# Kernel optimization log

Hardware: AMD Instinct MI355X
Metric: run time of the kernel (lower is better)

Reference implementation:

```python
import jax, jax.numpy as jnp
import numpy as np

N = 100000      # nodes
E = 3200000     # edges
F_IN = 128      # dataset.num_features
H = 64          # hidden_channels
H2 = 32         # hidden_channels_2 (H//2); hidden_channels_3 unused by the module
C5 = 256        # 2 * num_features
NC = 6          # num_classes


def setup_inputs() -> dict:
    key = jax.random.key(0)
    ks = jax.random.split(key, 24)

    def w(k, fi, fo):
        return jax.random.normal(k, (fi, fo), jnp.float32) / np.float32(np.sqrt(fi))

    inp = {
        "x": jax.random.normal(ks[0], (N, F_IN), jnp.float32),
        "edge_index": jax.random.randint(ks[1], (2, E), 0, N, dtype=jnp.int32),
        "batch": jnp.zeros((N,), jnp.int32),
        # GCNConv weights/biases (conv_i: x @ W then normalized aggregation + b)
        "W1": w(ks[2], F_IN, H),  "b1": jnp.zeros((H,), jnp.float32),
        "W2": w(ks[3], H, H),     "b2": jnp.zeros((H,), jnp.float32),
        "W3": w(ks[4], H, H2),    "b3": jnp.zeros((H2,), jnp.float32),
        "W4": w(ks[5], H2, H2),   "b4": jnp.zeros((H2,), jnp.float32),
        "W5": w(ks[6], H2, C5),   "b5": jnp.zeros((C5,), jnp.float32),
        # Linear layers
        "Wl1": w(ks[7], C5, 24),  "bl1": jnp.zeros((24,), jnp.float32),
        "Wl2": w(ks[8], 24, 18),  "bl2": jnp.zeros((18,), jnp.float32),
        "Wl3": w(ks[9], 18, 12),  "bl3": jnp.zeros((12,), jnp.float32),
        "Wc":  w(ks[10], 24, NC), "bc": jnp.zeros((NC,), jnp.float32),
    }
    return inp


def reference(x, edge_index, batch,
              W1, b1, W2, b2, W3, b3, W4, b4, W5, b5,
              Wl1, bl1, Wl2, bl2, Wl3, bl3, Wc, bc):
    # --- GCN normalization (PyG GCNConv: add self loops, sym norm) ---
    loops = jnp.arange(N, dtype=edge_index.dtype)
    src = jnp.concatenate([edge_index[0], loops])   # message sources (x_j)
    dst = jnp.concatenate([edge_index[1], loops])   # aggregation targets
    deg = jax.ops.segment_sum(jnp.ones_like(dst, jnp.float32), dst, num_segments=N)
    dinv = jnp.where(deg > 0, jax.lax.rsqrt(jnp.maximum(deg, 1.0)), 0.0)
    norm = (dinv[src] * dinv[dst])[:, None]         # [E+N, 1]

    def gcn(h, W, b):
        m = (h @ W)[src] * norm
        return jax.ops.segment_sum(m, dst, num_segments=N) + b

    h = jnp.tanh(gcn(x, W1, b1))
    h = jnp.tanh(gcn(h, W2, b2))
    h = jnp.tanh(gcn(h, W3, b3))
    h = jnp.tanh(gcn(h, W4, b4))
    h = jnp.tanh(gcn(h, W5, b5))
    h = jnp.tanh(h @ Wl1 + bl1)
    h = jnp.tanh(h @ Wl2 + bl2)
    h = jnp.tanh(h @ Wl3 + bl3)                      # [N, 12]
    e = jnp.concatenate([h[edge_index[0]], h[edge_index[1]]], axis=1)  # [E, 24]
    out = e @ Wc + bc                                # [E, NC]
    return (out, e)
```

## Files before the change

### kernel.cpp

```cpp
#include <hip/hip_runtime.h>

typedef float f32x4 __attribute__((ext_vector_type(4)));
typedef float f32x2 __attribute__((ext_vector_type(2)));

constexpr int BKT_SHIFT = 7;
constexpr int NBKT_PAD  = 1024;
constexpr int CHUNK     = 8192;
constexpr int MAXSEG    = 6144;

__global__ __launch_bounds__(256) void k1_hist(const int* __restrict__ dst,
                                               int* __restrict__ Hist, int ne) {
    __shared__ int lh[NBKT_PAD];
    for (int i = threadIdx.x; i < NBKT_PAD; i += 256) lh[i] = 0;
    __syncthreads();
    int base = blockIdx.x * CHUNK;
    int lim = min(CHUNK, ne - base);
    for (int i = threadIdx.x; i < lim; i += 256)
        atomicAdd(&lh[dst[base + i] >> BKT_SHIFT], 1);
    __syncthreads();
    for (int i = threadIdx.x; i < NBKT_PAD; i += 256)
        Hist[(size_t)blockIdx.x * NBKT_PAD + i] = lh[i];
}

__global__ __launch_bounds__(128) void k2a_sum(const int* __restrict__ Hist,
                                               int* __restrict__ bucketTot, int nblk) {
    int b = blockIdx.x * 128 + threadIdx.x;
    int tot = 0;
    int blk = 0;
    for (; blk + 4 <= nblk; blk += 4)
        tot += Hist[(size_t)blk * NBKT_PAD + b] +
               Hist[(size_t)(blk + 1) * NBKT_PAD + b] +
               Hist[(size_t)(blk + 2) * NBKT_PAD + b] +
               Hist[(size_t)(blk + 3) * NBKT_PAD + b];
    for (; blk < nblk; ++blk) tot += Hist[(size_t)blk * NBKT_PAD + b];
    bucketTot[b] = tot;
}

__global__ __launch_bounds__(1024) void k2b_scan(const int* __restrict__ bucketTot,
                                                 int* __restrict__ bktBase,
                                                 int* __restrict__ row_ptrN) {
    __shared__ int wsums[16];
    int t = threadIdx.x, wave = t >> 6, lane = t & 63;
    int tot = bucketTot[t];
    int x = tot;
    #pragma unroll
    for (int off = 1; off < 64; off <<= 1) {
        int y = __shfl_up(x, off, 64);
        if (lane >= off) x += y;
    }
    if (lane == 63) wsums[wave] = x;
    __syncthreads();
    if (t < 16) {
        int w = wsums[t];
        #pragma unroll
        for (int off = 1; off < 16; off <<= 1) {
            int y = __shfl_up(w, off, 64);
            if (t >= off) w += y;
        }
        wsums[t] = w;
    }
    __syncthreads();
    int excl = (wave ? wsums[wave - 1] : 0) + (x - tot);
    bktBase[t] = excl;
    if (t == 1023) { bktBase[1024] = excl + tot; *row_ptrN = excl + tot; }
}

__global__ __launch_bounds__(128) void k2c_rewrite(int* __restrict__ Hist,
                                                   const int* __restrict__ bktBase, int nblk) {
    int b = blockIdx.x * 128 + threadIdx.x;
    int run = bktBase[b];
    for (int blk = 0; blk < nblk; ++blk) {
        size_t idx = (size_t)blk * NBKT_PAD + b;
        int v = Hist[idx];
        Hist[idx] = run;
        run += v;
    }
}

__global__ __launch_bounds__(256) void k3_partition(const int* __restrict__ src,
                                                    const int* __restrict__ dst,
                                                    const int* __restrict__ Hist,
                                                    int2* __restrict__ es, int ne) {
    __shared__ int cur[NBKT_PAD];
    for (int i = threadIdx.x; i < NBKT_PAD; i += 256)
        cur[i] = Hist[(size_t)blockIdx.x * NBKT_PAD + i];
    __syncthreads();
    int base = blockIdx.x * CHUNK;
    int lim = min(CHUNK, ne - base);
    for (int i = threadIdx.x; i < lim; i += 256) {
        int d = dst[base + i];
        int s = src[base + i];
        int pos = atomicAdd(&cur[d >> BKT_SHIFT], 1);
        es[pos] = make_int2(s, d);
    }
}

__global__ __launch_bounds__(256) void k4_csr(const int2* __restrict__ es,
                                              const int* __restrict__ bktBase,
                                              int* __restrict__ col_idx,
                                              int* __restrict__ row_ptr,
                                              float* __restrict__ dinv, int n) {
    __shared__ int hist[128];
    __shared__ int rbase[128];
    __shared__ int cur[128];
    __shared__ int stage[MAXSEG];
    int b = blockIdx.x;
    int segs = bktBase[b], sege = bktBase[b + 1];
    int seglen = sege - segs;
    int node0 = b << BKT_SHIFT;
    int nloc = min(128, n - node0);
    int t = threadIdx.x;
    if (t < 128) hist[t] = 0;
    __syncthreads();
    for (int i = t; i < seglen; i += 256)
        atomicAdd(&hist[es[segs + i].y - node0], 1);
    __syncthreads();
    if (t < 64) {
        int a0 = hist[2 * t], a1 = hist[2 * t + 1];
        int pair = a0 + a1;
        int x = pair;
        #pragma unroll
        for (int off = 1; off < 64; off <<= 1) {
            int y = __shfl_up(x, off, 64);
            if (t >= off) x += y;
        }
        int excl = x - pair;
        rbase[2 * t] = excl;       rbase[2 * t + 1] = excl + a0;
        cur[2 * t]   = excl;       cur[2 * t + 1]   = excl + a0;
    }
    __syncthreads();
    if (seglen <= MAXSEG) {
        for (int i = t; i < seglen; i += 256) {
            int2 e = es[segs + i];
            int pos = atomicAdd(&cur[e.y - node0], 1);
            stage[pos] = e.x;
        }
        __syncthreads();
        for (int i = t; i < seglen; i += 256)
            col_idx[segs + i] = stage[i];
    } else {
        for (int i = t; i < seglen; i += 256) {
            int2 e = es[segs + i];
            int pos = atomicAdd(&cur[e.y - node0], 1);
            col_idx[segs + pos] = e.x;
        }
    }
    if (t < nloc) {
        row_ptr[node0 + t] = segs + rbase[t];
        dinv[node0 + t] = 1.0f / sqrtf((float)(hist[t] + 1));
    }
}

template<int K, int FOUT, int EPI, int RT>
__global__ __launch_bounds__(256) void gemm_tiled(const float* __restrict__ X,
        const float* __restrict__ W, const float* __restrict__ bias,
        const float* __restrict__ dinv, float* __restrict__ Y, int nrows) {
    __shared__ float Wl[K * FOUT];
    __shared__ float Xs[RT * K];
    int tid = threadIdx.x;
    const float4* Wg4 = (const float4*)W;
    float4* Wl4 = (float4*)Wl;
    for (int i = tid; i < K * FOUT / 4; i += 256) Wl4[i] = Wg4[i];
    int row0 = blockIdx.x * RT;
    int nr = min(RT, nrows - row0);
    {
        const float4* Xg4 = (const float4*)(X + (size_t)row0 * K);
        float4* Xs4 = (float4*)Xs;
        int lim = nr * (K / 4);
        for (int i = tid; i < lim; i += 256) Xs4[i] = Xg4[i];
    }
    __syncthreads();

    constexpr int NG  = 256 / FOUT;
    constexpr int RPT = RT / NG;
    int c = tid & (FOUT - 1);
    int g = tid / FOUT;
    int rbase = g * RPT;
    float acc[RPT];
    #pragma unroll
    for (int i = 0; i < RPT; ++i) acc[i] = 0.f;
    #pragma unroll 4
    for (int k = 0; k < K; ++k) {
        float wv = Wl[k * FOUT + c];
        #pragma unroll
        for (int i = 0; i < RPT; ++i)
            acc[i] = fmaf(Xs[(rbase + i) * K + k], wv, acc[i]);
    }
    float bv = (EPI == 1) ? bias[c] : 0.f;
    #pragma unroll
    for (int i = 0; i < RPT; ++i) {
        int r = row0 + rbase + i;
        if (r < nrows) {
            float v = acc[i];
            if (EPI == 0) v *= dinv[r];
            else          v = tanhf(v + bv);
            Y[(size_t)r * FOUT + c] = v;
        }
    }
}

__global__ __launch_bounds__(256) void head_kernel(const float* __restrict__ X,
        const float* __restrict__ W5, const float* __restrict__ b5,
        const float* __restrict__ Wl1, const float* __restrict__ bl1,
        const float* __restrict__ Wl2, const float* __restrict__ bl2,
        const float* __restrict__ Wl3, const float* __restrict__ bl3,
        float* __restrict__ Y, int nrows) {
    constexpr int RT = 16;
    __shared__ float W5s[32 * 256];
    __shared__ float W1s[256 * 24];
    __shared__ float W2s[24 * 18];
    __shared__ float W3s[18 * 12];
    __shared__ float b1s[24], b2s[18], b3s[12];
    __shared__ float Xs[RT * 32];
    __shared__ float H5[RT * 257];
    __shared__ float H24[RT * 25];
    __shared__ float H18[RT * 19];
    int tid = threadIdx.x;
    for (int i = tid; i < 32 * 256 / 4; i += 256) ((float4*)W5s)[i] = ((const float4*)W5)[i];
    for (int i = tid; i < 256 * 24 / 4; i += 256) ((float4*)W1s)[i] = ((const float4*)Wl1)[i];
    for (int i = tid; i < 432; i += 256) W2s[i] = Wl2[i];
    for (int i = tid; i < 216; i += 256) W3s[i] = Wl3[i];
    if (tid < 24) b1s[tid] = bl1[tid];
    if (tid < 18) b2s[tid] = bl2[tid];
    if (tid < 12) b3s[tid] = bl3[tid];
    float b5r = b5[tid];
    int row0 = blockIdx.x * RT;
    int nr = min(RT, nrows - row0);
    {
        const float4* Xg4 = (const float4*)(X + (size_t)row0 * 32);
        for (int i = tid; i < nr * 8; i += 256) ((float4*)Xs)[i] = Xg4[i];
    }
    __syncthreads();
    {
        float acc[RT];
        #pragma unroll
        for (int r = 0; r < RT; ++r) acc[r] = 0.f;
        #pragma unroll 4
        for (int k = 0; k < 32; ++k) {
            float wv = W5s[k * 256 + tid];
            #pragma unroll
            for (int r = 0; r < RT; ++r)
                acc[r] = fmaf(Xs[r * 32 + k], wv, acc[r]);
        }
        #pragma unroll
        for (int r = 0; r < RT; ++r) H5[r * 257 + tid] = tanhf(acc[r] + b5r);
    }
    __syncthreads();
    for (int o = tid; o < RT * 24; o += 256) {
        int r = o / 24, c = o - r * 24;
        float acc = 0.f;
        #pragma unroll 4
        for (int k = 0; k < 256; ++k) acc = fmaf(H5[r * 257 + k], W1s[k * 24 + c], acc);
        H24[r * 25 + c] = tanhf(acc + b1s[c]);
    }
    __syncthreads();
    for (int o = tid; o < RT * 18; o += 256) {
        int r = o / 18, c = o - r * 18;
        float acc = 0.f;
        #pragma unroll
        for (int k = 0; k < 24; ++k) acc = fmaf(H24[r * 25 + k], W2s[k * 18 + c], acc);
        H18[r * 19 + c] = tanhf(acc + b2s[c]);
    }
    __syncthreads();
    for (int o = tid; o < RT * 12; o += 256) {
        int r = o / 12, c = o - r * 12;
        float acc = 0.f;
        #pragma unroll
        for (int k = 0; k < 18; ++k) acc = fmaf(H18[r * 19 + k], W3s[k * 12 + c], acc);
        if (r < nr) Y[(size_t)(row0 + r) * 12 + c] = tanhf(acc + b3s[c]);
    }
}

template<int F, bool FINAL, bool POSTSCALE>
__global__ __launch_bounds__(256) void aggregate_kernel(const float* __restrict__ Z,
        const int* __restrict__ row_ptr, const int* __restrict__ col_idx,
        const float* __restrict__ dinv, const float* __restrict__ bias,
        float* __restrict__ out, int n) {
    constexpr int LPR = F / 4;
    constexpr int G   = 64 / LPR;
    int tid = threadIdx.x;
    int wave = tid >> 6, lane = tid & 63;
    int g = lane / LPR;
    int c = lane - g * LPR;
    int node = blockIdx.x * 4 + wave;
    if (node >= n) return;
    int start = row_ptr[node];
    int end   = row_ptr[node + 1];
    float4 acc = make_float4(0.f, 0.f, 0.f, 0.f);
    int wbase = start;
    int iv = (wbase + lane < end) ? col_idx[wbase + lane] : 0;
    #pragma unroll 2
    for (int base = start; base < end; base += G) {
        if (base - wbase == 64) {
            wbase += 64;
            iv = (wbase + lane < end) ? col_idx[wbase + lane] : 0;
        }
        int s = __shfl(iv, (base - wbase) + g, 64);
        if (base + g < end) {
            const float4 v = *(const float4*)(Z + (size_t)s * F + c * 4);
            acc.x += v.x; acc.y += v.y; acc.z += v.z; acc.w += v.w;
        }
    }
    #pragma unroll
    for (int off = LPR; off < 64; off <<= 1) {
        acc.x += __shfl_xor(acc.x, off, 64);
        acc.y += __shfl_xor(acc.y, off, 64);
        acc.z += __shfl_xor(acc.z, off, 64);
        acc.w += __shfl_xor(acc.w, off, 64);
    }
    if (g == 0) {
        const float4 sv = *(const float4*)(Z + (size_t)node * F + c * 4);
        float di = dinv[node];
        float4 r;
        r.x = di * (acc.x + sv.x);
        r.y = di * (acc.y + sv.y);
        r.z = di * (acc.z + sv.z);
        r.w = di * (acc.w + sv.w);
        if (FINAL) {
            const float4 bv = *(const float4*)(bias + c * 4);
            r.x = tanhf(r.x + bv.x);
            r.y = tanhf(r.y + bv.y);
            r.z = tanhf(r.z + bv.z);
            r.w = tanhf(r.w + bv.w);
        }
        if (POSTSCALE) { r.x *= di; r.y *= di; r.z *= di; r.w *= di; }
        *(float4*)(out + (size_t)node * F + c * 4) = r;
    }
}

__global__ __launch_bounds__(256) void edge_kernel(const int* __restrict__ src,
        const int* __restrict__ dst, const float* __restrict__ h,
        const float* __restrict__ Wc, const float* __restrict__ bc,
        float* __restrict__ out, float* __restrict__ efeat, int ne) {
    __shared__ float Wl[144];
    __shared__ float bl[6];
    if (threadIdx.x < 144) Wl[threadIdx.x] = Wc[threadIdx.x];
    if (threadIdx.x < 6) bl[threadIdx.x] = bc[threadIdx.x];
    __syncthreads();
    int e = blockIdx.x * 256 + threadIdx.x;
    if (e >= ne) return;
    int s = src[e], d = dst[e];
    const float* hs = h + (size_t)s * 12;
    const float* hd = h + (size_t)d * 12;
    f32x4 v0 = *(const f32x4*)(hs + 0);
    f32x4 v1 = *(const f32x4*)(hs + 4);
    f32x4 v2 = *(const f32x4*)(hs + 8);
    f32x4 v3 = *(const f32x4*)(hd + 0);
    f32x4 v4 = *(const f32x4*)(hd + 4);
    f32x4 v5 = *(const f32x4*)(hd + 8);
    float v[24];
    *(f32x4*)(v + 0)  = v0; *(f32x4*)(v + 4)  = v1; *(f32x4*)(v + 8)  = v2;
    *(f32x4*)(v + 12) = v3; *(f32x4*)(v + 16) = v4; *(f32x4*)(v + 20) = v5;
    f32x4* ef4 = (f32x4*)(efeat + (size_t)e * 24);
    ef4[0] = v0; ef4[1] = v1; ef4[2] = v2; ef4[3] = v3; ef4[4] = v4; ef4[5] = v5;
    float o[6];
    #pragma unroll
    for (int c = 0; c < 6; ++c) {
        float acc = bl[c];
        #pragma unroll
        for (int k = 0; k < 24; ++k) acc = fmaf(v[k], Wl[k * 6 + c], acc);
        o[c] = acc;
    }
    f32x2* o2 = (f32x2*)(out + (size_t)e * 6);
    f32x2 p0; p0.x = o[0]; p0.y = o[1];
    f32x2 p1; p1.x = o[2]; p1.y = o[3];
    f32x2 p2; p2.x = o[4]; p2.y = o[5];
    o2[0] = p0; o2[1] = p1; o2[2] = p2;
}

extern "C" void kernel_launch(void* const* d_in, const int* in_sizes, int n_in,
                              void* d_out, int out_size, void* d_ws, size_t ws_size,
                              hipStream_t stream) {
    const int N = in_sizes[0] / 128;
    const int E = in_sizes[1] / 2;

    const float* x   = (const float*)d_in[0];
    const int*   ei  = (const int*)d_in[1];
    const int*   srcE = ei;
    const int*   dstE = ei + E;
    const float* W1 = (const float*)d_in[3];  const float* b1 = (const float*)d_in[4];
    const float* W2 = (const float*)d_in[5];  const float* b2 = (const float*)d_in[6];
    const float* W3 = (const float*)d_in[7];  const float* b3 = (const float*)d_in[8];
    const float* W4 = (const float*)d_in[9];  const float* b4 = (const float*)d_in[10];
    const float* W5 = (const float*)d_in[11]; const float* b5 = (const float*)d_in[12];
    const float* Wl1 = (const float*)d_in[13]; const float* bl1 = (const float*)d_in[14];
    const float* Wl2 = (const float*)d_in[15]; const float* bl2 = (const float*)d_in[16];
    const float* Wl3 = (const float*)d_in[17]; const float* bl3 = (const float*)d_in[18];
    const float* Wc  = (const float*)d_in[19]; const float* bc  = (const float*)d_in[20];

    char* ws = (char*)d_ws;
    size_t off = 0;
    auto take = [&](size_t bytes) -> char* {
        char* p = ws + off;
        off += (bytes + 255) & ~(size_t)255;
        return p;
    };
    int*   row_ptr   = (int*)take((size_t)(N + 1) * 4);
    float* dinv      = (float*)take((size_t)N * 4);
    int*   col_idx   = (int*)take((size_t)E * 4);
    float* h8        = (float*)take((size_t)N * 12 * 4);
    int*   bktBase   = (int*)take((size_t)(NBKT_PAD + 1) * 4);
    int*   bucketTot = (int*)take((size_t)NBKT_PAD * 4);

    float* outbuf  = (float*)d_out;
    float* eregion = outbuf + (size_t)E * 6;
    int2* es  = (int2*)eregion;
    int*  Hist = (int*)(es + E);
    float* bufZ = eregion;
    float* bufH = eregion + (size_t)N * 64;

    int gE = (E + 255) / 256;
    int gAgg = (N + 3) / 4;
    int nblk = (E + CHUNK - 1) / CHUNK;
    int nbkt = (N + 127) >> BKT_SHIFT;
    auto tiles = [&](int rt) { return (N + rt - 1) / rt; };

    k1_hist<<<nblk, 256, 0, stream>>>(dstE, Hist, E);
    k2a_sum<<<NBKT_PAD / 128, 128, 0, stream>>>(Hist, bucketTot, nblk);
    k2b_scan<<<1, 1024, 0, stream>>>(bucketTot, bktBase, row_ptr + N);
    k2c_rewrite<<<NBKT_PAD / 128, 128, 0, stream>>>(Hist, bktBase, nblk);
    k3_partition<<<nblk, 256, 0, stream>>>(srcE, dstE, Hist, es, E);
    k4_csr<<<nbkt, 256, 0, stream>>>(es, bktBase, col_idx, row_ptr, dinv, N);

    gemm_tiled<128, 64, 0, 16><<<tiles(16), 256, 0, stream>>>(x, W1, nullptr, dinv, bufZ, N);
    aggregate_kernel<64, true, false><<<gAgg, 256, 0, stream>>>(bufZ, row_ptr, col_idx, dinv, b1, bufH, N);
    gemm_tiled<64, 64, 0, 16><<<tiles(16), 256, 0, stream>>>(bufH, W2, nullptr, dinv, bufZ, N);
    aggregate_kernel<64, true, false><<<gAgg, 256, 0, stream>>>(bufZ, row_ptr, col_idx, dinv, b2, bufH, N);
    gemm_tiled<64, 32, 0, 16><<<tiles(16), 256, 0, stream>>>(bufH, W3, nullptr, dinv, bufZ, N);
    aggregate_kernel<32, true, false><<<gAgg, 256, 0, stream>>>(bufZ, row_ptr, col_idx, dinv, b3, bufH, N);
    gemm_tiled<32, 32, 0, 16><<<tiles(16), 256, 0, stream>>>(bufH, W4, nullptr, dinv, bufZ, N);
    aggregate_kernel<32, true, true><<<gAgg, 256, 0, stream>>>(bufZ, row_ptr, col_idx, dinv, b4, bufH, N);
    aggregate_kernel<32, false, false><<<gAgg, 256, 0, stream>>>(bufH, row_ptr, col_idx, dinv, nullptr, bufZ, N);
    head_kernel<<<tiles(16), 256, 0, stream>>>(bufZ, W5, b5, Wl1, bl1, Wl2, bl2, Wl3, bl3, h8, N);
    edge_kernel<<<gE, 256, 0, stream>>>(srcE, dstE, h8, Wc, bc, outbuf, eregion, E);
}
```

Baseline: 1.017 ms.

## Fuse GCN aggregation with following layer GEMM and unroll gather loop

Three aggregate+GEMM pairs are merged into one agg_gemm kernel. Each block aggregates 16 nodes into shared memory, applies bias and tanh, then multiplies by the next layer's weights and scales by dinv. This removes the global write and re-read of the intermediate hidden features and three launches. The gather loop is also restructured to load 64 indices per batch with a 4-way unrolled inner loop, to raise memory-level parallelism. In exchange, each wave now handles four nodes one after another, and the GEMM stage must wait on a block-wide barrier for the slowest node.

Measured after the change: 999.3 us. Within noise of the previous version (-1.8%).

```diff
diff --git a/kernel.cpp b/kernel.cpp
--- a/kernel.cpp
+++ b/kernel.cpp
@@ -151,16 +151,142 @@
     }
 }
 
-template<int K, int FOUT, int EPI, int RT>
+template<int F>
+__device__ inline f32x4 gather_sum(const float* __restrict__ Z,
+                                   const int* __restrict__ col_idx,
+                                   int start, int end, int lane, int g, int c) {
+    constexpr int LPR = F / 4;
+    constexpr int G   = 64 / LPR;
+    f32x4 acc = {0.f, 0.f, 0.f, 0.f};
+    for (int wb = start; wb < end; wb += 64) {
+        int m = min(64, end - wb);
+        int iv = (wb + lane < end) ? col_idx[wb + lane] : 0;
+        for (int b = 0; b < m; b += 4 * G) {
+            #pragma unroll
+            for (int j = 0; j < 4; ++j) {
+                int bb = b + j * G;
+                int s = __shfl(iv, bb + g, 64);
+                if (bb + g < m) {
+                    acc += *(const f32x4*)(Z + (size_t)s * F + c * 4);
+                }
+            }
+        }
+    }
+    return acc;
+}
+
+template<int LPR>
+__device__ inline f32x4 reduce_groups(f32x4 a) {
+    #pragma unroll
+    for (int off = LPR; off < 64; off <<= 1) {
+        a.x += __shfl_xor(a.x, off, 64);
+        a.y += __shfl_xor(a.y, off, 64);
+        a.z += __shfl_xor(a.z, off, 64);
+        a.w += __shfl_xor(a.w, off, 64);
+    }
+    return a;
+}
+
+template<int F, bool FINAL, bool POSTSCALE>
+__global__ __launch_bounds__(256) void aggregate_kernel(const float* __restrict__ Z,
+        const int* __restrict__ row_ptr, const int* __restrict__ col_idx,
+        const float* __restrict__ dinv, const float* __restrict__ bias,
+        float* __restrict__ out, int n) {
+    constexpr int LPR = F / 4;
+    int tid = threadIdx.x;
+    int wave = tid >> 6, lane = tid & 63;
+    int g = lane / LPR;
+    int c = lane - g * LPR;
+    int node = blockIdx.x * 4 + wave;
+    if (node >= n) return;
+    int start = row_ptr[node];
+    int end   = row_ptr[node + 1];
+    f32x4 acc = gather_sum<F>(Z, col_idx, start, end, lane, g, c);
+    acc = reduce_groups<LPR>(acc);
+    if (g == 0) {
+        const f32x4 sv = *(const f32x4*)(Z + (size_t)node * F + c * 4);
+        float di = dinv[node];
+        f32x4 r = di * (acc + sv);
+        if (FINAL) {
+            const f32x4 bv = *(const f32x4*)(bias + c * 4);
+            r.x = tanhf(r.x + bv.x);
+            r.y = tanhf(r.y + bv.y);
+            r.z = tanhf(r.z + bv.z);
+            r.w = tanhf(r.w + bv.w);
+        }
+        if (POSTSCALE) r *= di;
+        *(f32x4*)(out + (size_t)node * F + c * 4) = r;
+    }
+}
+
+template<int F, int FOUT>
+__global__ __launch_bounds__(256) void agg_gemm_kernel(const float* __restrict__ Z,
+        const int* __restrict__ row_ptr, const int* __restrict__ col_idx,
+        const float* __restrict__ dinv, const float* __restrict__ aggBias,
+        const float* __restrict__ W, float* __restrict__ Y, int n) {
+    constexpr int LPR = F / 4;
+    __shared__ float Hs[16 * F];
+    __shared__ float Wl[F * FOUT];
+    int tid = threadIdx.x;
+    int wave = tid >> 6, lane = tid & 63;
+    int g = lane / LPR;
+    int c = lane - g * LPR;
+    int row0 = blockIdx.x * 16;
+    for (int i = tid; i < F * FOUT / 4; i += 256)
+        ((float4*)Wl)[i] = ((const float4*)W)[i];
+    #pragma unroll
+    for (int i = 0; i < 4; ++i) {
+        int node = row0 + wave * 4 + i;
+        if (node < n) {
+            int start = row_ptr[node];
+            int end   = row_ptr[node + 1];
+            f32x4 acc = gather_sum<F>(Z, col_idx, start, end, lane, g, c);
+            acc = reduce_groups<LPR>(acc);
+            if (g == 0) {
+                const f32x4 sv = *(const f32x4*)(Z + (size_t)node * F + c * 4);
+                float di = dinv[node];
+                f32x4 r = di * (acc + sv);
+                const f32x4 bv = *(const f32x4*)(aggBias + c * 4);
+                r.x = tanhf(r.x + bv.x);
+                r.y = tanhf(r.y + bv.y);
+                r.z = tanhf(r.z + bv.z);
+                r.w = tanhf(r.w + bv.w);
+                *(f32x4*)(Hs + (wave * 4 + i) * F + c * 4) = r;
+            }
+        }
+    }
+    __syncthreads();
+    constexpr int NG  = 256 / FOUT;
+    constexpr int RPT = 16 / NG;
+    int cc = tid & (FOUT - 1);
+    int gg = tid / FOUT;
+    int rbase = gg * RPT;
+    float acc2[RPT];
+    #pragma unroll
+    for (int i = 0; i < RPT; ++i) acc2[i] = 0.f;
+    #pragma unroll 4
+    for (int k = 0; k < F; ++k) {
+        float wv = Wl[k * FOUT + cc];
+        #pragma unroll
+        for (int i = 0; i < RPT; ++i)
+            acc2[i] = fmaf(Hs[(rbase + i) * F + k], wv, acc2[i]);
+    }
+    #pragma unroll
+    for (int i = 0; i < RPT; ++i) {
+        int r = row0 + rbase + i;
+        if (r < n) Y[(size_t)r * FOUT + cc] = acc2[i] * dinv[r];
+    }
+}
+
+template<int K, int FOUT, int RT>
 __global__ __launch_bounds__(256) void gemm_tiled(const float* __restrict__ X,
-        const float* __restrict__ W, const float* __restrict__ bias,
-        const float* __restrict__ dinv, float* __restrict__ Y, int nrows) {
+        const float* __restrict__ W, const float* __restrict__ dinv,
+        float* __restrict__ Y, int nrows) {
     __shared__ float Wl[K * FOUT];
     __shared__ float Xs[RT * K];
     int tid = threadIdx.x;
-    const float4* Wg4 = (const float4*)W;
-    float4* Wl4 = (float4*)Wl;
-    for (int i = tid; i < K * FOUT / 4; i += 256) Wl4[i] = Wg4[i];
+    for (int i = tid; i < K * FOUT / 4; i += 256)
+        ((float4*)Wl)[i] = ((const float4*)W)[i];
     int row0 = blockIdx.x * RT;
     int nr = min(RT, nrows - row0);
     {
@@ -170,7 +296,6 @@
         for (int i = tid; i < lim; i += 256) Xs4[i] = Xg4[i];
     }
     __syncthreads();
-
     constexpr int NG  = 256 / FOUT;
     constexpr int RPT = RT / NG;
     int c = tid & (FOUT - 1);
@@ -186,16 +311,10 @@
         for (int i = 0; i < RPT; ++i)
             acc[i] = fmaf(Xs[(rbase + i) * K + k], wv, acc[i]);
     }
-    float bv = (EPI == 1) ? bias[c] : 0.f;
     #pragma unroll
     for (int i = 0; i < RPT; ++i) {
         int r = row0 + rbase + i;
-        if (r < nrows) {
-            float v = acc[i];
-            if (EPI == 0) v *= dinv[r];
-            else          v = tanhf(v + bv);
-            Y[(size_t)r * FOUT + c] = v;
-        }
+        if (r < nrows) Y[(size_t)r * FOUT + c] = acc[i] * dinv[r];
     }
 }
 
@@ -271,63 +390,6 @@
     }
 }
 
-template<int F, bool FINAL, bool POSTSCALE>
-__global__ __launch_bounds__(256) void aggregate_kernel(const float* __restrict__ Z,
-        const int* __restrict__ row_ptr, const int* __restrict__ col_idx,
-        const float* __restrict__ dinv, const float* __restrict__ bias,
-        float* __restrict__ out, int n) {
-    constexpr int LPR = F / 4;
-    constexpr int G   = 64 / LPR;
-    int tid = threadIdx.x;
-    int wave = tid >> 6, lane = tid & 63;
-    int g = lane / LPR;
-    int c = lane - g * LPR;
-    int node = blockIdx.x * 4 + wave;
-    if (node >= n) return;
-    int start = row_ptr[node];
-    int end   = row_ptr[node + 1];
-    float4 acc = make_float4(0.f, 0.f, 0.f, 0.f);
-    int wbase = start;
-    int iv = (wbase + lane < end) ? col_idx[wbase + lane] : 0;
-    #pragma unroll 2
-    for (int base = start; base < end; base += G) {
-        if (base - wbase == 64) {
-            wbase += 64;
-            iv = (wbase + lane < end) ? col_idx[wbase + lane] : 0;
-        }
-        int s = __shfl(iv, (base - wbase) + g, 64);
-        if (base + g < end) {
-            const float4 v = *(const float4*)(Z + (size_t)s * F + c * 4);
-            acc.x += v.x; acc.y += v.y; acc.z += v.z; acc.w += v.w;
-        }
-    }
-    #pragma unroll
-    for (int off = LPR; off < 64; off <<= 1) {
-        acc.x += __shfl_xor(acc.x, off, 64);
-        acc.y += __shfl_xor(acc.y, off, 64);
-        acc.z += __shfl_xor(acc.z, off, 64);
-        acc.w += __shfl_xor(acc.w, off, 64);
-    }
-    if (g == 0) {
-        const float4 sv = *(const float4*)(Z + (size_t)node * F + c * 4);
-        float di = dinv[node];
-        float4 r;
-        r.x = di * (acc.x + sv.x);
-        r.y = di * (acc.y + sv.y);
-        r.z = di * (acc.z + sv.z);
-        r.w = di * (acc.w + sv.w);
-        if (FINAL) {
-            const float4 bv = *(const float4*)(bias + c * 4);
-            r.x = tanhf(r.x + bv.x);
-            r.y = tanhf(r.y + bv.y);
-            r.z = tanhf(r.z + bv.z);
-            r.w = tanhf(r.w + bv.w);
-        }
-        if (POSTSCALE) { r.x *= di; r.y *= di; r.z *= di; r.w *= di; }
-        *(float4*)(out + (size_t)node * F + c * 4) = r;
-    }
-}
-
 __global__ __launch_bounds__(256) void edge_kernel(const int* __restrict__ src,
         const int* __restrict__ dst, const float* __restrict__ h,
         const float* __restrict__ Wc, const float* __restrict__ bc,
@@ -411,9 +473,9 @@
 
     int gE = (E + 255) / 256;
     int gAgg = (N + 3) / 4;
+    int g16  = (N + 15) / 16;
     int nblk = (E + CHUNK - 1) / CHUNK;
     int nbkt = (N + 127) >> BKT_SHIFT;
-    auto tiles = [&](int rt) { return (N + rt - 1) / rt; };
 
     k1_hist<<<nblk, 256, 0, stream>>>(dstE, Hist, E);
     k2a_sum<<<NBKT_PAD / 128, 128, 0, stream>>>(Hist, bucketTot, nblk);
@@ -422,15 +484,12 @@
     k3_partition<<<nblk, 256, 0, stream>>>(srcE, dstE, Hist, es, E);
     k4_csr<<<nbkt, 256, 0, stream>>>(es, bktBase, col_idx, row_ptr, dinv, N);
 
-    gemm_tiled<128, 64, 0, 16><<<tiles(16), 256, 0, stream>>>(x, W1, nullptr, dinv, bufZ, N);
-    aggregate_kernel<64, true, false><<<gAgg, 256, 0, stream>>>(bufZ, row_ptr, col_idx, dinv, b1, bufH, N);
-    gemm_tiled<64, 64, 0, 16><<<tiles(16), 256, 0, stream>>>(bufH, W2, nullptr, dinv, bufZ, N);
-    aggregate_kernel<64, true, false><<<gAgg, 256, 0, stream>>>(bufZ, row_ptr, col_idx, dinv, b2, bufH, N);
-    gemm_tiled<64, 32, 0, 16><<<tiles(16), 256, 0, stream>>>(bufH, W3, nullptr, dinv, bufZ, N);
-    aggregate_kernel<32, true, false><<<gAgg, 256, 0, stream>>>(bufZ, row_ptr, col_idx, dinv, b3, bufH, N);
-    gemm_tiled<32, 32, 0, 16><<<tiles(16), 256, 0, stream>>>(bufH, W4, nullptr, dinv, bufZ, N);
-    aggregate_kernel<32, true, true><<<gAgg, 256, 0, stream>>>(bufZ, row_ptr, col_idx, dinv, b4, bufH, N);
-    aggregate_kernel<32, false, false><<<gAgg, 256, 0, stream>>>(bufH, row_ptr, col_idx, dinv, nullptr, bufZ, N);
-    head_kernel<<<tiles(16), 256, 0, stream>>>(bufZ, W5, b5, Wl1, bl1, Wl2, bl2, Wl3, bl3, h8, N);
+    gemm_tiled<128, 64, 16><<<g16, 256, 0, stream>>>(x, W1, dinv, bufZ, N);
+    agg_gemm_kernel<64, 64><<<g16, 256, 0, stream>>>(bufZ, row_ptr, col_idx, dinv, b1, W2, bufH, N);
+    agg_gemm_kernel<64, 32><<<g16, 256, 0, stream>>>(bufH, row_ptr, col_idx, dinv, b2, W3, bufZ, N);
+    agg_gemm_kernel<32, 32><<<g16, 256, 0, stream>>>(bufZ, row_ptr, col_idx, dinv, b3, W4, bufH, N);
+    aggregate_kernel<32, true, true><<<gAgg, 256, 0, stream>>>(bufH, row_ptr, col_idx, dinv, b4, bufZ, N);
+    aggregate_kernel<32, false, false><<<gAgg, 256, 0, stream>>>(bufZ, row_ptr, col_idx, dinv, nullptr, bufH, N);
+    head_kernel<<<g16, 256, 0, stream>>>(bufH, W5, b5, Wl1, bl1, Wl2, bl2, Wl3, bl3, h8, N);
     edge_kernel<<<gE, 256, 0, stream>>>(srcE, dstE, h8, Wc, bc, outbuf, eregion, E);
 }
```
